# Optimization experiments

Measured on AMD Instinct MI355X. Metric: run time of the kernel, lower is better.

The kernel has to match this reference:

```python
import jax, jax.numpy as jnp
import numpy as np

DIM = 512        # model dim
MOE_DIM = 256    # expert hidden dim
E = 64           # n_routed experts
G = 8            # n_routed_group
TOPK_G = 4       # n_topk_group
K = 8            # n_experts_per_tok
SCALE = 2.5      # routed_scale
CAP = 1024


def setup_inputs() -> dict:
    key = jax.random.key(0)
    ks = jax.random.split(key, 6)
    x = jax.random.normal(ks[0], (4, 512, DIM), jnp.float32)
    gate_w = jax.random.normal(ks[1], (E, DIM), jnp.float32) / np.sqrt(DIM).astype(np.float32)
    gate_b = jax.random.normal(ks[2], (E,), jnp.float32) * 0.01
    w1 = jax.random.normal(ks[3], (E, DIM, MOE_DIM), jnp.float32) / np.sqrt(DIM).astype(np.float32)
    w3 = jax.random.normal(ks[4], (E, DIM, MOE_DIM), jnp.float32) / np.sqrt(DIM).astype(np.float32)
    w2 = jax.random.normal(ks[5], (E, MOE_DIM, DIM), jnp.float32) / np.sqrt(MOE_DIM).astype(np.float32)
    return {"x": x, "gate_w": gate_w, "gate_b": gate_b, "w1": w1, "w3": w3, "w2": w2}


def _gate(x2, gate_w, gate_b):
    # x2: [T, DIM] -> (weights [T,K], indices [T,K])
    T = x2.shape[0]
    scores = jax.nn.sigmoid(x2 @ gate_w.T)                      # [T, E]
    s = (scores + gate_b).reshape(T, G, E // G)                  # grouped scores
    group_scores = jax.lax.top_k(s, 2)[0].sum(-1)                # [T, G] sum of top-2 per group
    top_groups = jax.lax.top_k(group_scores, TOPK_G)[1]          # [T, TOPK_G]
    gmask = jnp.zeros((T, G), bool).at[jnp.arange(T)[:, None], top_groups].set(True)
    s = jnp.where(gmask[..., None], s, -jnp.inf).reshape(T, E)
    idx = jax.lax.top_k(s, K)[1]                                 # [T, K]
    w = jnp.take_along_axis(scores, idx, axis=1)                 # original (pre-bias) scores
    w = w / w.sum(-1, keepdims=True) * SCALE
    return w, idx


def _moe_forward(x, gate_w, gate_b, w1, w3, w2):
    shape = x.shape
    x2 = x.reshape(-1, DIM)                                      # [T, DIM]
    T = x2.shape[0]
    w, idx = _gate(x2, gate_w, gate_b)
    flat_e = idx.reshape(-1)                                     # [T*K]
    # position of each (token, slot) within its expert's buffer, in order
    oh = (flat_e[:, None] == jnp.arange(E)[None, :]).astype(jnp.int32)  # [T*K, E]
    pos = (jnp.cumsum(oh, axis=0) * oh).sum(-1) - 1              # [T*K]
    x_rep = jnp.repeat(x2, K, axis=0)                            # [T*K, DIM]
    # dispatch into per-expert buffers [E, CAP, DIM]
    xb = jnp.zeros((E, CAP, DIM), x2.dtype).at[flat_e, pos].set(x_rep, mode='drop')
    h = jax.nn.silu(jnp.einsum('ecd,edm->ecm', xb, w1)) * jnp.einsum('ecd,edm->ecm', xb, w3)
    yb = jnp.einsum('ecm,emd->ecd', h, w2)                       # [E, CAP, DIM]
    # combine: gather back and weight
    y = yb.at[flat_e, pos].get(mode='fill', fill_value=0.0) * w.reshape(-1)[:, None]
    return y.reshape(T, K, DIM).sum(1).reshape(shape)


def reference(x, gate_w, gate_b, w1, w3, w2):
    return _moe_forward(x, gate_w, gate_b, w1, w3, w2)
```

## Files before the change

### kernel.cpp

```cpp
#include <hip/hip_runtime.h>

#define T_TOK 2048
#define DIM   512
#define MOE   256
#define NE    64
#define NG    8
#define TOPKG 4
#define TOPK  8
#define CAP   1024
#define MOE_SCALE 2.5f

typedef float f32x4 __attribute__((ext_vector_type(4)));
typedef short s16x8 __attribute__((ext_vector_type(8)));

__device__ __forceinline__ unsigned short f2bf(float f) {
    unsigned u = __builtin_bit_cast(unsigned, f);
    unsigned r = (u + 0x7fffu + ((u >> 16) & 1u)) >> 16;
    return (unsigned short)r;
}
__device__ __forceinline__ unsigned pk2(float lo, float hi) {
    return (unsigned)f2bf(lo) | ((unsigned)f2bf(hi) << 16);
}

__global__ __launch_bounds__(256) void gwt_k(const float* __restrict__ gw,
                                             float* __restrict__ gwT)
{
    int idx = blockIdx.x * 256 + threadIdx.x;
    int e = idx >> 9, k = idx & 511;
    gwT[(size_t)(k >> 2) * 256 + e * 4 + (k & 3)] = gw[idx];
}

__global__ __launch_bounds__(256) void gate_fused_k(const float* __restrict__ x,
                                                    const float* __restrict__ gwT,
                                                    const float* __restrict__ gb,
                                                    int* __restrict__ counts,
                                                    int* __restrict__ etok,
                                                    float* __restrict__ wt_of,
                                                    short* __restrict__ xb)
{
    __shared__ float xs[4][512];
    int w = threadIdx.x >> 6, lane = threadIdx.x & 63;
    int t = blockIdx.x * 4 + w;

    {
        const float4* xr = (const float4*)(x + (size_t)t * DIM);
        float4 v0 = xr[lane * 2], v1 = xr[lane * 2 + 1];
        *(float4*)&xs[w][lane * 8]     = v0;
        *(float4*)&xs[w][lane * 8 + 4] = v1;
        short o[8];
        o[0] = (short)f2bf(v0.x); o[1] = (short)f2bf(v0.y);
        o[2] = (short)f2bf(v0.z); o[3] = (short)f2bf(v0.w);
        o[4] = (short)f2bf(v1.x); o[5] = (short)f2bf(v1.y);
        o[6] = (short)f2bf(v1.z); o[7] = (short)f2bf(v1.w);
        *(s16x8*)(xb + (size_t)t * DIM + lane * 8) = *(const s16x8*)o;
    }
    __syncthreads();

    const float4* gt = (const float4*)gwT;
    float a0 = 0.f, a1 = 0.f, a2 = 0.f, a3 = 0.f;
#pragma unroll 4
    for (int k4 = 0; k4 < 128; k4 += 4) {
        float4 g0 = gt[(k4 + 0) * 64 + lane];
        float4 g1 = gt[(k4 + 1) * 64 + lane];
        float4 g2 = gt[(k4 + 2) * 64 + lane];
        float4 g3 = gt[(k4 + 3) * 64 + lane];
        float4 x0 = *(const float4*)&xs[w][(k4 + 0) * 4];
        float4 x1 = *(const float4*)&xs[w][(k4 + 1) * 4];
        float4 x2 = *(const float4*)&xs[w][(k4 + 2) * 4];
        float4 x3 = *(const float4*)&xs[w][(k4 + 3) * 4];
        a0 += g0.x * x0.x + g0.y * x0.y + g0.z * x0.z + g0.w * x0.w;
        a1 += g1.x * x1.x + g1.y * x1.y + g1.z * x1.z + g1.w * x1.w;
        a2 += g2.x * x2.x + g2.y * x2.y + g2.z * x2.z + g2.w * x2.w;
        a3 += g3.x * x3.x + g3.y * x3.y + g3.z * x3.z + g3.w * x3.w;
    }
    float acc = (a0 + a1) + (a2 + a3);
    float sc = 1.f / (1.f + __expf(-acc));
    float s  = sc + gb[lane];

    float m1 = s, m2 = -1e30f;
#pragma unroll
    for (int d = 1; d < 8; d <<= 1) {
        float o1 = __shfl_xor(m1, d);
        float o2 = __shfl_xor(m2, d);
        float n1 = fmaxf(m1, o1);
        float n2 = fmaxf(fminf(m1, o1), fmaxf(m2, o2));
        m1 = n1; m2 = n2;
    }
    float gv = m1 + m2;

    bool gkeep = false;
#pragma unroll
    for (int it = 0; it < TOPKG; ++it) {
        float m = gv;
#pragma unroll
        for (int d = 1; d < 64; d <<= 1) m = fmaxf(m, __shfl_xor(m, d));
        unsigned long long mask = __ballot(gv == m);
        int ldr = __ffsll(mask) - 1;
        if ((lane >> 3) == (ldr >> 3)) { gkeep = true; gv = -2e30f; }
    }
    float sv = gkeep ? s : -1e30f;

    float wsum = 0.f;
    int my_e = 0; float my_w = 0.f;
#pragma unroll
    for (int k = 0; k < TOPK; ++k) {
        float m = sv;
#pragma unroll
        for (int d = 1; d < 64; d <<= 1) m = fmaxf(m, __shfl_xor(m, d));
        unsigned long long mask = __ballot(sv == m);
        int l = __ffsll(mask) - 1;
        float wk = __shfl(sc, l);
        wsum += wk;
        if (lane == k) { my_e = l; my_w = wk; }
        if (lane == l) sv = -2e30f;
    }
    float scale = MOE_SCALE / wsum;
    if (lane < TOPK) {
        int p = atomicAdd(&counts[my_e], 1);
        int rid = t * TOPK + lane;
        bool ok = (p < CAP);
        if (ok) etok[my_e * CAP + p] = rid;
        wt_of[rid] = ok ? my_w * scale : 0.f;
    }
}

__global__ __launch_bounds__(64) void scan_k(const int* __restrict__ counts,
                                             int* __restrict__ tbase)
{
    int lane = threadIdx.x;
    int ne = min(counts[lane], CAP);
    int nt = (ne + 31) >> 5;
    int v = nt;
#pragma unroll
    for (int d = 1; d < 64; d <<= 1) {
        int o = __shfl_up(v, d);
        if (lane >= d) v += o;
    }
    tbase[lane] = v - nt;
}

__global__ __launch_bounds__(256) void gather_k(const short* __restrict__ xb,
                                                const int* __restrict__ counts,
                                                const int* __restrict__ etok,
                                                const int* __restrict__ tbase,
                                                short* __restrict__ xgf)
{
    int e = blockIdx.x >> 3, sub3 = blockIdx.x & 7;
    int w = threadIdx.x >> 6, lane = threadIdx.x & 63;
    int T = sub3 * 4 + w;
    int ne = min(counts[e], CAP);
    int nt = (ne + 31) >> 5;
    if (T >= nt) return;
    int G = tbase[e] + T;
    int q = lane >> 4, m16 = lane & 15;
    int r0 = T * 32 + m16, r1 = T * 32 + 16 + m16;
    bool ok0 = r0 < ne, ok1 = r1 < ne;
    int tok0 = ok0 ? (etok[e * CAP + r0] >> 3) : 0;
    int tok1 = ok1 ? (etok[e * CAP + r1] >> 3) : 0;
    const short* s0 = xb + (size_t)tok0 * DIM + q * 8;
    const short* s1 = xb + (size_t)tok1 * DIM + q * 8;
    short* dst = xgf + (size_t)G * 32 * 512 + lane * 8;
    s16x8 z = {0, 0, 0, 0, 0, 0, 0, 0};
#pragma unroll
    for (int kt = 0; kt < 16; ++kt) {
        s16x8 a0 = ok0 ? *(const s16x8*)(s0 + kt * 32) : z;
        s16x8 a1 = ok1 ? *(const s16x8*)(s1 + kt * 32) : z;
        *(s16x8*)(dst + (size_t)(kt * 2 + 0) * 512) = a0;
        *(s16x8*)(dst + (size_t)(kt * 2 + 1) * 512) = a1;
    }
}

__global__ __launch_bounds__(256) void gemm1_k(const short* __restrict__ xgf,
                                               const float* __restrict__ w1,
                                               const float* __restrict__ w3,
                                               const int* __restrict__ counts,
                                               const int* __restrict__ tbase,
                                               short* __restrict__ hgf)
{
    __shared__ short Bl[2][2][16][64][8];
    __shared__ short Ct[4][16][34];

    int e  = blockIdx.x & 63, cg = blockIdx.x >> 6;
    int n0 = cg * 32;
    int tid = threadIdx.x;
    int w = tid >> 6, lane = tid & 63;
    int q = lane >> 4, m16 = lane & 15;

    const float* W1e = w1 + (size_t)e * DIM * MOE + n0;
    const float* W3e = w3 + (size_t)e * DIM * MOE + n0;
#pragma unroll
    for (int it = 0; it < 8; ++it) {
        int idx = it * 256 + tid;
        int r2  = idx >> 3;
        int cq  = (idx & 7) * 4;
        int k   = r2 * 2;
        int kt = k >> 5, qq = (k >> 3) & 3, j0 = k & 7;
        int s = cq >> 4, c15 = cq & 15;
        const float* p1 = W1e + (size_t)k * MOE + cq;
        const float* p3 = W3e + (size_t)k * MOE + cq;
        float4 lo1 = *(const float4*)p1;
        float4 hi1 = *(const float4*)(p1 + MOE);
        float4 lo3 = *(const float4*)p3;
        float4 hi3 = *(const float4*)(p3 + MOE);
        unsigned* b0 = (unsigned*)&Bl[0][s][kt][qq * 16 + c15][j0];
        b0[0]  = pk2(lo1.x, hi1.x);
        b0[4]  = pk2(lo1.y, hi1.y);
        b0[8]  = pk2(lo1.z, hi1.z);
        b0[12] = pk2(lo1.w, hi1.w);
        unsigned* b1 = (unsigned*)&Bl[1][s][kt][qq * 16 + c15][j0];
        b1[0]  = pk2(lo3.x, hi3.x);
        b1[4]  = pk2(lo3.y, hi3.y);
        b1[8]  = pk2(lo3.z, hi3.z);
        b1[12] = pk2(lo3.w, hi3.w);
    }
    __syncthreads();

    int ne = min(counts[e], CAP);
    int nt = (ne + 31) >> 5;
    int G0 = tbase[e];
    short* ct = &Ct[w][0][0];

    for (int T = w; T < nt; T += 4) {
        const short* A = xgf + (size_t)(G0 + T) * 32 * 512 + lane * 8;

        f32x4 g0[2], g1[2], u0[2], u1[2];
#pragma unroll
        for (int s = 0; s < 2; ++s) {
            g0[s] = (f32x4)0.f; g1[s] = (f32x4)0.f;
            u0[s] = (f32x4)0.f; u1[s] = (f32x4)0.f;
        }
#pragma unroll
        for (int kt = 0; kt < 16; ++kt) {
            s16x8 a0 = *(const s16x8*)(A + (size_t)(kt * 2 + 0) * 512);
            s16x8 a1 = *(const s16x8*)(A + (size_t)(kt * 2 + 1) * 512);
#pragma unroll
            for (int s = 0; s < 2; ++s) {
                s16x8 b1 = *(const s16x8*)&Bl[0][s][kt][lane][0];
                g0[s] = __builtin_amdgcn_mfma_f32_16x16x32_bf16(a0, b1, g0[s], 0, 0, 0);
                g1[s] = __builtin_amdgcn_mfma_f32_16x16x32_bf16(a1, b1, g1[s], 0, 0, 0);
                s16x8 b3 = *(const s16x8*)&Bl[1][s][kt][lane][0];
                u0[s] = __builtin_amdgcn_mfma_f32_16x16x32_bf16(a0, b3, u0[s], 0, 0, 0);
                u1[s] = __builtin_amdgcn_mfma_f32_16x16x32_bf16(a1, b3, u1[s], 0, 0, 0);
            }
        }
#pragma unroll
        for (int sub = 0; sub < 2; ++sub) {
#pragma unroll
            for (int s = 0; s < 2; ++s)
#pragma unroll
                for (int r = 0; r < 4; ++r) {
                    float g = sub ? g1[s][r] : g0[s][r];
                    float uu = sub ? u1[s][r] : u0[s][r];
                    float hv = g / (1.f + __expf(-g)) * uu;
                    ct[(q * 4 + r) * 34 + s * 16 + m16] = (short)f2bf(hv);
                }
            s16x8 hv8 = *(const s16x8*)&ct[m16 * 34 + q * 8];
            *(s16x8*)(hgf + (size_t)(((G0 + T) * 8 + cg) * 2 + sub) * 512 + lane * 8) = hv8;
        }
    }
}

__global__ __launch_bounds__(256) void gemm2_k(const short* __restrict__ hgf,
                                               const float* __restrict__ w2,
                                               const int* __restrict__ counts,
                                               const int* __restrict__ etok,
                                               const int* __restrict__ tbase,
                                               short* __restrict__ ybuf)
{
    __shared__ short Bl[4][8][64][8];

    int e  = blockIdx.x & 63, cg = blockIdx.x >> 6;
    int n0 = cg * 64;
    int tid = threadIdx.x;
    int w = tid >> 6, lane = tid & 63;
    int q = lane >> 4, m16 = lane & 15;

    const float* W2e = w2 + (size_t)e * MOE * DIM + n0;
#pragma unroll
    for (int it = 0; it < 8; ++it) {
        int idx = it * 256 + tid;
        int r2  = idx >> 4;
        int cq  = (idx & 15) * 4;
        int k   = r2 * 2;
        int kt = k >> 5, qq = (k >> 3) & 3, j0 = k & 7;
        int s = cq >> 4, c15 = cq & 15;
        const float* p2 = W2e + (size_t)k * DIM + cq;
        float4 lo = *(const float4*)p2;
        float4 hi = *(const float4*)(p2 + DIM);
        unsigned* b = (unsigned*)&Bl[s][kt][qq * 16 + c15][j0];
        b[0]  = pk2(lo.x, hi.x);
        b[4]  = pk2(lo.y, hi.y);
        b[8]  = pk2(lo.z, hi.z);
        b[12] = pk2(lo.w, hi.w);
    }
    __syncthreads();

    int ne = min(counts[e], CAP);
    int nt = (ne + 31) >> 5;
    int G0 = tbase[e];
    const int* el = etok + e * CAP;

    for (int T = w; T < nt; T += 4) {
        const short* A = hgf + (size_t)(G0 + T) * 16 * 512 + lane * 8;

        f32x4 y0[4], y1[4];
#pragma unroll
        for (int s = 0; s < 4; ++s) { y0[s] = (f32x4)0.f; y1[s] = (f32x4)0.f; }
#pragma unroll
        for (int kt = 0; kt < 8; ++kt) {
            s16x8 a0 = *(const s16x8*)(A + (size_t)(kt * 2 + 0) * 512);
            s16x8 a1 = *(const s16x8*)(A + (size_t)(kt * 2 + 1) * 512);
#pragma unroll
            for (int s = 0; s < 4; ++s) {
                s16x8 b = *(const s16x8*)&Bl[s][kt][lane][0];
                y0[s] = __builtin_amdgcn_mfma_f32_16x16x32_bf16(a0, b, y0[s], 0, 0, 0);
                y1[s] = __builtin_amdgcn_mfma_f32_16x16x32_bf16(a1, b, y1[s], 0, 0, 0);
            }
        }
#pragma unroll
        for (int s = 0; s < 4; ++s)
#pragma unroll
            for (int r = 0; r < 4; ++r) {
                int row0 = T * 32 + q * 4 + r;
                if (row0 < ne)
                    ybuf[(size_t)el[row0] * DIM + n0 + s * 16 + m16] = (short)f2bf(y0[s][r]);
                int row1 = row0 + 16;
                if (row1 < ne)
                    ybuf[(size_t)el[row1] * DIM + n0 + s * 16 + m16] = (short)f2bf(y1[s][r]);
            }
    }
}

__global__ __launch_bounds__(256) void combine_k(const short* __restrict__ ybuf,
                                                 const float* __restrict__ wt_of,
                                                 float* __restrict__ out)
{
    int t = blockIdx.x;
    int tid = threadIdx.x;
    const int* yb = (const int*)ybuf;
    float sx = 0.f, sy = 0.f;
#pragma unroll
    for (int k = 0; k < TOPK; ++k) {
        float wk = wt_of[t * TOPK + k];
        int v = yb[(size_t)(t * TOPK + k) * (DIM / 2) + tid];
        float lo = __builtin_bit_cast(float, (unsigned)v << 16);
        float hi = __builtin_bit_cast(float, (unsigned)v & 0xffff0000u);
        sx += wk * lo;
        sy += wk * hi;
    }
    float2 o = {sx, sy};
    ((float2*)out)[(size_t)t * (DIM / 2) + tid] = o;
}

extern "C" void kernel_launch(void* const* d_in, const int* in_sizes, int n_in,
                              void* d_out, int out_size, void* d_ws, size_t ws_size,
                              hipStream_t stream)
{
    const float* x  = (const float*)d_in[0];
    const float* gw = (const float*)d_in[1];
    const float* gb = (const float*)d_in[2];
    const float* w1 = (const float*)d_in[3];
    const float* w3 = (const float*)d_in[4];
    const float* w2 = (const float*)d_in[5];

    char* ws = (char*)d_ws;
    short* xb    = (short*)(ws);
    short* xgf   = (short*)(ws + 2097152);
    short* hgf   = (short*)(ws + 20971520);
    short* ybuf  = (short*)(ws + 30408704);
    float* gwT   = (float*)(ws + 47185920);
    int*   etok  = (int*)  (ws + 47316992);
    float* wt_of = (float*)(ws + 47579136);
    int*   counts= (int*)  (ws + 47644672);
    int*   tbase = (int*)  (ws + 47644928);

    hipMemsetAsync(counts, 0, NE * 4, stream);

    gwt_k<<<128, 256, 0, stream>>>(gw, gwT);
    gate_fused_k<<<T_TOK / 4, 256, 0, stream>>>(x, gwT, gb, counts, etok, wt_of, xb);
    scan_k<<<1, 64, 0, stream>>>(counts, tbase);
    gather_k<<<NE * 8, 256, 0, stream>>>(xb, counts, etok, tbase, xgf);
    gemm1_k<<<NE * 8, 256, 0, stream>>>(xgf, w1, w3, counts, tbase, hgf);
    gemm2_k<<<NE * 8, 256, 0, stream>>>(hgf, w2, counts, etok, tbase, ybuf);
    combine_k<<<T_TOK, 256, 0, stream>>>(ybuf, wt_of, (float*)d_out);
}
```

Measured before the change: 277.0 us.

## Halve GEMM column tiles, double grid, and process two row tiles per wave

Both expert GEMM kernels now cover half as many output columns per block (16 for gemm1, 32 for gemm2) and launch twice as many blocks. This cuts the shared-memory weight tile and raises occupancy. Each wave now handles two 32-row token tiles at once so every B fragment read from LDS feeds more MFMAs. The gather kernel batches its loads before its stores, and launch bounds request 4 blocks per CU. The trade-off is that each expert's weights are read and converted by twice as many blocks, and per-wave work becomes less balanced.

```diff
diff --git a/kernel.cpp b/kernel.cpp
--- a/kernel.cpp
+++ b/kernel.cpp
@@ -139,11 +139,11 @@
     tbase[lane] = v - nt;
 }
 
-__global__ __launch_bounds__(256) void gather_k(const short* __restrict__ xb,
-                                                const int* __restrict__ counts,
-                                                const int* __restrict__ etok,
-                                                const int* __restrict__ tbase,
-                                                short* __restrict__ xgf)
+__global__ __launch_bounds__(256, 4) void gather_k(const short* __restrict__ xb,
+                                                   const int* __restrict__ counts,
+                                                   const int* __restrict__ etok,
+                                                   const int* __restrict__ tbase,
+                                                   short* __restrict__ xgf)
 {
     int e = blockIdx.x >> 3, sub3 = blockIdx.x & 7;
     int w = threadIdx.x >> 6, lane = threadIdx.x & 63;
@@ -159,26 +159,127 @@
     int tok1 = ok1 ? (etok[e * CAP + r1] >> 3) : 0;
     const short* s0 = xb + (size_t)tok0 * DIM + q * 8;
     const short* s1 = xb + (size_t)tok1 * DIM + q * 8;
-    short* dst = xgf + (size_t)G * 32 * 512 + lane * 8;
+    short* dst = xgf + (size_t)G * 16384 + lane * 8;
     s16x8 z = {0, 0, 0, 0, 0, 0, 0, 0};
 #pragma unroll
-    for (int kt = 0; kt < 16; ++kt) {
-        s16x8 a0 = ok0 ? *(const s16x8*)(s0 + kt * 32) : z;
-        s16x8 a1 = ok1 ? *(const s16x8*)(s1 + kt * 32) : z;
-        *(s16x8*)(dst + (size_t)(kt * 2 + 0) * 512) = a0;
-        *(s16x8*)(dst + (size_t)(kt * 2 + 1) * 512) = a1;
-    }
-}
-
-__global__ __launch_bounds__(256) void gemm1_k(const short* __restrict__ xgf,
-                                               const float* __restrict__ w1,
-                                               const float* __restrict__ w3,
-                                               const int* __restrict__ counts,
-                                               const int* __restrict__ tbase,
-                                               short* __restrict__ hgf)
-{
-    __shared__ short Bl[2][2][16][64][8];
-    __shared__ short Ct[4][16][34];
+    for (int b4 = 0; b4 < 4; ++b4) {
+        s16x8 v[8];
+#pragma unroll
+        for (int i = 0; i < 4; ++i) {
+            int kt = b4 * 4 + i;
+            v[i * 2]     = ok0 ? *(const s16x8*)(s0 + kt * 32) : z;
+            v[i * 2 + 1] = ok1 ? *(const s16x8*)(s1 + kt * 32) : z;
+        }
+#pragma unroll
+        for (int i = 0; i < 4; ++i) {
+            int kt = b4 * 4 + i;
+            *(s16x8*)(dst + (size_t)(kt * 2 + 0) * 512) = v[i * 2];
+            *(s16x8*)(dst + (size_t)(kt * 2 + 1) * 512) = v[i * 2 + 1];
+        }
+    }
+}
+
+__global__ __launch_bounds__(256, 4) void gemm1_k(const short* __restrict__ xgf,
+                                                  const float* __restrict__ w1,
+                                                  const float* __restrict__ w3,
+                                                  const int* __restrict__ counts,
+                                                  const int* __restrict__ tbase,
+                                                  short* __restrict__ hgf)
+{
+    __shared__ short Bl[2][16][64][8];
+    __shared__ short Ct[4][2][16][24];
+
+    int e  = blockIdx.x & 63, cg = blockIdx.x >> 6;
+    int n0 = cg * 16;
+    int tid = threadIdx.x;
+    int w = tid >> 6, lane = tid & 63;
+    int q = lane >> 4, m16 = lane & 15;
+
+    const float* W1e = w1 + (size_t)e * DIM * MOE + n0;
+    const float* W3e = w3 + (size_t)e * DIM * MOE + n0;
+#pragma unroll
+    for (int it = 0; it < 8; ++it) {
+        int idx = it * 256 + tid;
+        int mat = idx >> 10;
+        int rem = idx & 1023;
+        int r2  = rem >> 2;
+        int cq  = (rem & 3) * 4;
+        int k   = r2 * 2;
+        int kt = k >> 5, qf = (k >> 3) & 3, j0 = k & 7;
+        const float* p = (mat ? W3e : W1e) + (size_t)k * MOE + cq;
+        float4 lo = *(const float4*)p;
+        float4 hi = *(const float4*)(p + MOE);
+        unsigned* b = (unsigned*)&Bl[mat][kt][qf * 16 + cq][j0];
+        b[0]  = pk2(lo.x, hi.x);
+        b[4]  = pk2(lo.y, hi.y);
+        b[8]  = pk2(lo.z, hi.z);
+        b[12] = pk2(lo.w, hi.w);
+    }
+    __syncthreads();
+
+    int ne = min(counts[e], CAP);
+    int nt = (ne + 31) >> 5;
+    int G0 = tbase[e];
+
+    for (int T0 = w * 2; T0 < nt; T0 += 8) {
+        bool v1 = (T0 + 1) < nt;
+        const short* A0 = xgf + (size_t)(G0 + T0) * 16384 + lane * 8;
+        const short* A1 = xgf + (size_t)(G0 + (v1 ? T0 + 1 : T0)) * 16384 + lane * 8;
+
+        f32x4 acc[2][2][2];
+#pragma unroll
+        for (int i = 0; i < 2; ++i)
+#pragma unroll
+            for (int j = 0; j < 2; ++j)
+#pragma unroll
+                for (int m = 0; m < 2; ++m) acc[i][j][m] = (f32x4)0.f;
+
+#pragma unroll
+        for (int kt = 0; kt < 16; ++kt) {
+            s16x8 a00 = *(const s16x8*)(A0 + (size_t)(kt * 2 + 0) * 512);
+            s16x8 a01 = *(const s16x8*)(A0 + (size_t)(kt * 2 + 1) * 512);
+            s16x8 a10 = *(const s16x8*)(A1 + (size_t)(kt * 2 + 0) * 512);
+            s16x8 a11 = *(const s16x8*)(A1 + (size_t)(kt * 2 + 1) * 512);
+            s16x8 b1 = *(const s16x8*)&Bl[0][kt][lane][0];
+            s16x8 b3 = *(const s16x8*)&Bl[1][kt][lane][0];
+            acc[0][0][0] = __builtin_amdgcn_mfma_f32_16x16x32_bf16(a00, b1, acc[0][0][0], 0, 0, 0);
+            acc[0][1][0] = __builtin_amdgcn_mfma_f32_16x16x32_bf16(a01, b1, acc[0][1][0], 0, 0, 0);
+            acc[1][0][0] = __builtin_amdgcn_mfma_f32_16x16x32_bf16(a10, b1, acc[1][0][0], 0, 0, 0);
+            acc[1][1][0] = __builtin_amdgcn_mfma_f32_16x16x32_bf16(a11, b1, acc[1][1][0], 0, 0, 0);
+            acc[0][0][1] = __builtin_amdgcn_mfma_f32_16x16x32_bf16(a00, b3, acc[0][0][1], 0, 0, 0);
+            acc[0][1][1] = __builtin_amdgcn_mfma_f32_16x16x32_bf16(a01, b3, acc[0][1][1], 0, 0, 0);
+            acc[1][0][1] = __builtin_amdgcn_mfma_f32_16x16x32_bf16(a10, b3, acc[1][0][1], 0, 0, 0);
+            acc[1][1][1] = __builtin_amdgcn_mfma_f32_16x16x32_bf16(a11, b3, acc[1][1][1], 0, 0, 0);
+        }
+
+#pragma unroll
+        for (int t2 = 0; t2 < 2; ++t2) {
+            if (t2 && !v1) break;
+#pragma unroll
+            for (int sub = 0; sub < 2; ++sub)
+#pragma unroll
+                for (int r = 0; r < 4; ++r) {
+                    float g = acc[t2][sub][0][r];
+                    float u = acc[t2][sub][1][r];
+                    float hv = g / (1.f + __expf(-g)) * u;
+                    Ct[w][sub][q * 4 + r][m16] = (short)f2bf(hv);
+                }
+            int sub = q >> 1;
+            s16x8 hv8 = *(const s16x8*)&Ct[w][sub][m16][(q & 1) * 8];
+            size_t slot = ((size_t)(G0 + T0 + t2) * 8 + (cg >> 1)) * 2 + sub;
+            *(s16x8*)(hgf + slot * 512 + ((cg & 1) * 2 + (q & 1)) * 128 + m16 * 8) = hv8;
+        }
+    }
+}
+
+__global__ __launch_bounds__(256, 4) void gemm2_k(const short* __restrict__ hgf,
+                                                  const float* __restrict__ w2,
+                                                  const int* __restrict__ counts,
+                                                  const int* __restrict__ etok,
+                                                  const int* __restrict__ tbase,
+                                                  short* __restrict__ ybuf)
+{
+    __shared__ short Bl[2][8][64][8];
 
     int e  = blockIdx.x & 63, cg = blockIdx.x >> 6;
     int n0 = cg * 32;
@@ -186,108 +287,19 @@
     int w = tid >> 6, lane = tid & 63;
     int q = lane >> 4, m16 = lane & 15;
 
-    const float* W1e = w1 + (size_t)e * DIM * MOE + n0;
-    const float* W3e = w3 + (size_t)e * DIM * MOE + n0;
-#pragma unroll
-    for (int it = 0; it < 8; ++it) {
+    const float* W2e = w2 + (size_t)e * MOE * DIM + n0;
+#pragma unroll
+    for (int it = 0; it < 4; ++it) {
         int idx = it * 256 + tid;
         int r2  = idx >> 3;
         int cq  = (idx & 7) * 4;
         int k   = r2 * 2;
-        int kt = k >> 5, qq = (k >> 3) & 3, j0 = k & 7;
+        int kt2 = k >> 5, qf = (k >> 3) & 3, j0 = k & 7;
         int s = cq >> 4, c15 = cq & 15;
-        const float* p1 = W1e + (size_t)k * MOE + cq;
-        const float* p3 = W3e + (size_t)k * MOE + cq;
-        float4 lo1 = *(const float4*)p1;
-        float4 hi1 = *(const float4*)(p1 + MOE);
-        float4 lo3 = *(const float4*)p3;
-        float4 hi3 = *(const float4*)(p3 + MOE);
-        unsigned* b0 = (unsigned*)&Bl[0][s][kt][qq * 16 + c15][j0];
-        b0[0]  = pk2(lo1.x, hi1.x);
-        b0[4]  = pk2(lo1.y, hi1.y);
-        b0[8]  = pk2(lo1.z, hi1.z);
-        b0[12] = pk2(lo1.w, hi1.w);
-        unsigned* b1 = (unsigned*)&Bl[1][s][kt][qq * 16 + c15][j0];
-        b1[0]  = pk2(lo3.x, hi3.x);
-        b1[4]  = pk2(lo3.y, hi3.y);
-        b1[8]  = pk2(lo3.z, hi3.z);
-        b1[12] = pk2(lo3.w, hi3.w);
-    }
-    __syncthreads();
-
-    int ne = min(counts[e], CAP);
-    int nt = (ne + 31) >> 5;
-    int G0 = tbase[e];
-    short* ct = &Ct[w][0][0];
-
-    for (int T = w; T < nt; T += 4) {
-        const short* A = xgf + (size_t)(G0 + T) * 32 * 512 + lane * 8;
-
-        f32x4 g0[2], g1[2], u0[2], u1[2];
-#pragma unroll
-        for (int s = 0; s < 2; ++s) {
-            g0[s] = (f32x4)0.f; g1[s] = (f32x4)0.f;
-            u0[s] = (f32x4)0.f; u1[s] = (f32x4)0.f;
-        }
-#pragma unroll
-        for (int kt = 0; kt < 16; ++kt) {
-            s16x8 a0 = *(const s16x8*)(A + (size_t)(kt * 2 + 0) * 512);
-            s16x8 a1 = *(const s16x8*)(A + (size_t)(kt * 2 + 1) * 512);
-#pragma unroll
-            for (int s = 0; s < 2; ++s) {
-                s16x8 b1 = *(const s16x8*)&Bl[0][s][kt][lane][0];
-                g0[s] = __builtin_amdgcn_mfma_f32_16x16x32_bf16(a0, b1, g0[s], 0, 0, 0);
-                g1[s] = __builtin_amdgcn_mfma_f32_16x16x32_bf16(a1, b1, g1[s], 0, 0, 0);
-                s16x8 b3 = *(const s16x8*)&Bl[1][s][kt][lane][0];
-                u0[s] = __builtin_amdgcn_mfma_f32_16x16x32_bf16(a0, b3, u0[s], 0, 0, 0);
-                u1[s] = __builtin_amdgcn_mfma_f32_16x16x32_bf16(a1, b3, u1[s], 0, 0, 0);
-            }
-        }
-#pragma unroll
-        for (int sub = 0; sub < 2; ++sub) {
-#pragma unroll
-            for (int s = 0; s < 2; ++s)
-#pragma unroll
-                for (int r = 0; r < 4; ++r) {
-                    float g = sub ? g1[s][r] : g0[s][r];
-                    float uu = sub ? u1[s][r] : u0[s][r];
-                    float hv = g / (1.f + __expf(-g)) * uu;
-                    ct[(q * 4 + r) * 34 + s * 16 + m16] = (short)f2bf(hv);
-                }
-            s16x8 hv8 = *(const s16x8*)&ct[m16 * 34 + q * 8];
-            *(s16x8*)(hgf + (size_t)(((G0 + T) * 8 + cg) * 2 + sub) * 512 + lane * 8) = hv8;
-        }
-    }
-}
-
-__global__ __launch_bounds__(256) void gemm2_k(const short* __restrict__ hgf,
-                                               const float* __restrict__ w2,
-                                               const int* __restrict__ counts,
-                                               const int* __restrict__ etok,
-                                               const int* __restrict__ tbase,
-                                               short* __restrict__ ybuf)
-{
-    __shared__ short Bl[4][8][64][8];
-
-    int e  = blockIdx.x & 63, cg = blockIdx.x >> 6;
-    int n0 = cg * 64;
-    int tid = threadIdx.x;
-    int w = tid >> 6, lane = tid & 63;
-    int q = lane >> 4, m16 = lane & 15;
-
-    const float* W2e = w2 + (size_t)e * MOE * DIM + n0;
-#pragma unroll
-    for (int it = 0; it < 8; ++it) {
-        int idx = it * 256 + tid;
-        int r2  = idx >> 4;
-        int cq  = (idx & 15) * 4;
-        int k   = r2 * 2;
-        int kt = k >> 5, qq = (k >> 3) & 3, j0 = k & 7;
-        int s = cq >> 4, c15 = cq & 15;
-        const float* p2 = W2e + (size_t)k * DIM + cq;
-        float4 lo = *(const float4*)p2;
-        float4 hi = *(const float4*)(p2 + DIM);
-        unsigned* b = (unsigned*)&Bl[s][kt][qq * 16 + c15][j0];
+        const float* p = W2e + (size_t)k * DIM + cq;
+        float4 lo = *(const float4*)p;
+        float4 hi = *(const float4*)(p + DIM);
+        unsigned* b = (unsigned*)&Bl[s][kt2][qf * 16 + c15][j0];
         b[0]  = pk2(lo.x, hi.x);
         b[4]  = pk2(lo.y, hi.y);
         b[8]  = pk2(lo.z, hi.z);
@@ -300,34 +312,53 @@
     int G0 = tbase[e];
     const int* el = etok + e * CAP;
 
-    for (int T = w; T < nt; T += 4) {
-        const short* A = hgf + (size_t)(G0 + T) * 16 * 512 + lane * 8;
-
-        f32x4 y0[4], y1[4];
-#pragma unroll
-        for (int s = 0; s < 4; ++s) { y0[s] = (f32x4)0.f; y1[s] = (f32x4)0.f; }
+    for (int T0 = w * 2; T0 < nt; T0 += 8) {
+        bool v1 = (T0 + 1) < nt;
+        const short* A0 = hgf + (size_t)(G0 + T0) * 8192 + lane * 8;
+        const short* A1 = hgf + (size_t)(G0 + (v1 ? T0 + 1 : T0)) * 8192 + lane * 8;
+
+        f32x4 acc[2][2][2];
+#pragma unroll
+        for (int i = 0; i < 2; ++i)
+#pragma unroll
+            for (int j = 0; j < 2; ++j)
+#pragma unroll
+                for (int m = 0; m < 2; ++m) acc[i][j][m] = (f32x4)0.f;
+
 #pragma unroll
         for (int kt = 0; kt < 8; ++kt) {
-            s16x8 a0 = *(const s16x8*)(A + (size_t)(kt * 2 + 0) * 512);
-            s16x8 a1 = *(const s16x8*)(A + (size_t)(kt * 2 + 1) * 512);
-#pragma unroll
-            for (int s = 0; s < 4; ++s) {
-                s16x8 b = *(const s16x8*)&Bl[s][kt][lane][0];
-                y0[s] = __builtin_amdgcn_mfma_f32_16x16x32_bf16(a0, b, y0[s], 0, 0, 0);
-                y1[s] = __builtin_amdgcn_mfma_f32_16x16x32_bf16(a1, b, y1[s], 0, 0, 0);
-            }
-        }
-#pragma unroll
-        for (int s = 0; s < 4; ++s)
-#pragma unroll
-            for (int r = 0; r < 4; ++r) {
-                int row0 = T * 32 + q * 4 + r;
-                if (row0 < ne)
-                    ybuf[(size_t)el[row0] * DIM + n0 + s * 16 + m16] = (short)f2bf(y0[s][r]);
-                int row1 = row0 + 16;
-                if (row1 < ne)
-                    ybuf[(size_t)el[row1] * DIM + n0 + s * 16 + m16] = (short)f2bf(y1[s][r]);
-            }
+            s16x8 a00 = *(const s16x8*)(A0 + (size_t)(kt * 2 + 0) * 512);
+            s16x8 a01 = *(const s16x8*)(A0 + (size_t)(kt * 2 + 1) * 512);
+            s16x8 a10 = *(const s16x8*)(A1 + (size_t)(kt * 2 + 0) * 512);
+            s16x8 a11 = *(const s16x8*)(A1 + (size_t)(kt * 2 + 1) * 512);
+            s16x8 b0 = *(const s16x8*)&Bl[0][kt][lane][0];
+            s16x8 b1 = *(const s16x8*)&Bl[1][kt][lane][0];
+            acc[0][0][0] = __builtin_amdgcn_mfma_f32_16x16x32_bf16(a00, b0, acc[0][0][0], 0, 0, 0);
+            acc[0][1][0] = __builtin_amdgcn_mfma_f32_16x16x32_bf16(a01, b0, acc[0][1][0], 0, 0, 0);
+            acc[1][0][0] = __builtin_amdgcn_mfma_f32_16x16x32_bf16(a10, b0, acc[1][0][0], 0, 0, 0);
+            acc[1][1][0] = __builtin_amdgcn_mfma_f32_16x16x32_bf16(a11, b0, acc[1][1][0], 0, 0, 0);
+            acc[0][0][1] = __builtin_amdgcn_mfma_f32_16x16x32_bf16(a00, b1, acc[0][0][1], 0, 0, 0);
+            acc[0][1][1] = __builtin_amdgcn_mfma_f32_16x16x32_bf16(a01, b1, acc[0][1][1], 0, 0, 0);
+            acc[1][0][1] = __builtin_amdgcn_mfma_f32_16x16x32_bf16(a10, b1, acc[1][0][1], 0, 0, 0);
+            acc[1][1][1] = __builtin_amdgcn_mfma_f32_16x16x32_bf16(a11, b1, acc[1][1][1], 0, 0, 0);
+        }
+
+#pragma unroll
+        for (int t2 = 0; t2 < 2; ++t2) {
+            if (t2 && !v1) break;
+            int T = T0 + t2;
+#pragma unroll
+            for (int sub = 0; sub < 2; ++sub)
+#pragma unroll
+                for (int s = 0; s < 2; ++s)
+#pragma unroll
+                    for (int r = 0; r < 4; ++r) {
+                        int row = T * 32 + sub * 16 + q * 4 + r;
+                        if (row < ne)
+                            ybuf[(size_t)el[row] * DIM + n0 + s * 16 + m16] =
+                                (short)f2bf(acc[t2][sub][s][r]);
+                    }
+        }
     }
 }
 
@@ -380,7 +411,7 @@
     gate_fused_k<<<T_TOK / 4, 256, 0, stream>>>(x, gwT, gb, counts, etok, wt_of, xb);
     scan_k<<<1, 64, 0, stream>>>(counts, tbase);
     gather_k<<<NE * 8, 256, 0, stream>>>(xb, counts, etok, tbase, xgf);
-    gemm1_k<<<NE * 8, 256, 0, stream>>>(xgf, w1, w3, counts, tbase, hgf);
-    gemm2_k<<<NE * 8, 256, 0, stream>>>(hgf, w2, counts, etok, tbase, ybuf);
+    gemm1_k<<<NE * 16, 256, 0, stream>>>(xgf, w1, w3, counts, tbase, hgf);
+    gemm2_k<<<NE * 16, 256, 0, stream>>>(hgf, w2, counts, etok, tbase, ybuf);
     combine_k<<<T_TOK, 256, 0, stream>>>(ybuf, wt_of, (float*)d_out);
 }
```

Result: no change. 280.9 us (+1.4%).
